# Performance work log

Hardware: AMD Instinct MI355X
Metric: run time of the kernel (lower is better)

Reference implementation:

```python
import jax, jax.numpy as jnp
import numpy as np

D = 2048; HQ = 16; HKV = 4; HD = 128
E = 8; F = 2048; FS = 11008; TOPK = 2
B = 2; S = 1024
EPS = 1e-6
NEG = -1e9


def setup_inputs() -> dict:
    key = jax.random.key(0)
    ks = jax.random.split(key, 16)
    p = lambda k, shape: jax.random.normal(k, shape, jnp.float32) * 0.02
    # rotary tables (rotate-half convention): [S, HD]
    pos = jnp.arange(S, dtype=jnp.float32)[:, None]
    inv = 1.0 / (10000.0 ** (jnp.arange(0, HD, 2, dtype=jnp.float32) / HD))
    ang = pos * inv[None, :]
    cos = jnp.concatenate([jnp.cos(ang), jnp.cos(ang)], axis=-1)
    sin = jnp.concatenate([jnp.sin(ang), jnp.sin(ang)], axis=-1)
    return dict(
        x=jax.random.normal(ks[0], (B, S, D), jnp.float32),
        rope_cos=cos, rope_sin=sin,
        attn_norm_w=jnp.ones((D,), jnp.float32),
        ffn_norm_w=jnp.ones((D,), jnp.float32),
        wq=p(ks[1], (D, HQ * HD)), bq=jnp.zeros((HQ * HD,), jnp.float32),
        wk=p(ks[2], (D, HKV * HD)), bk=jnp.zeros((HKV * HD,), jnp.float32),
        wv=p(ks[3], (D, HKV * HD)), bv=jnp.zeros((HKV * HD,), jnp.float32),
        wo=p(ks[4], (HQ * HD, D)),
        router_w=p(ks[5], (D, E)),
        w_gate=p(ks[6], (E, D, F)), w_up=p(ks[7], (E, D, F)), w_down=p(ks[8], (E, F, D)),
        ws_gate=p(ks[9], (D, FS)), ws_up=p(ks[10], (D, FS)), ws_down=p(ks[11], (FS, D)),
    )


def rmsnorm(x, w):
    return x * jax.lax.rsqrt(jnp.mean(x * x, axis=-1, keepdims=True) + EPS) * w


def rotate_half(x):
    x1, x2 = jnp.split(x, 2, axis=-1)
    return jnp.concatenate([-x2, x1], axis=-1)


def reference(x, rope_cos, rope_sin, attn_norm_w, ffn_norm_w,
              wq, bq, wk, bk, wv, bv, wo, router_w,
              w_gate, w_up, w_down, ws_gate, ws_up, ws_down):
    b, s, d = x.shape
    # ---- attention sublayer ----
    h = rmsnorm(x, attn_norm_w)
    q = (h @ wq + bq).reshape(b, s, HQ, HD)
    k = (h @ wk + bk).reshape(b, s, HKV, HD)
    v = (h @ wv + bv).reshape(b, s, HKV, HD)
    cos = rope_cos[None, :, None, :]
    sin = rope_sin[None, :, None, :]
    q = q * cos + rotate_half(q) * sin
    k = k * cos + rotate_half(k) * sin
    rep = HQ // HKV
    k = jnp.repeat(k, rep, axis=2)   # [b,s,HQ,HD]
    v = jnp.repeat(v, rep, axis=2)
    scores = jnp.einsum('bqhd,bkhd->bhqk', q, k) / np.sqrt(HD).astype(np.float32)
    causal = jnp.tril(jnp.ones((s, s), bool))
    scores = jnp.where(causal[None, None], scores, NEG)
    attn = jax.nn.softmax(scores, axis=-1)
    o = jnp.einsum('bhqk,bkhd->bqhd', attn, v).reshape(b, s, HQ * HD) @ wo
    new_k, new_v = k, v
    x = x + o
    # ---- MoE sublayer ----
    hn = rmsnorm(x, ffn_norm_w).reshape(b * s, d)   # [T,D]
    logits = hn @ router_w                           # [T,E]
    probs = jax.nn.softmax(logits, axis=-1)
    topv, topi = jax.lax.top_k(probs, TOPK)          # [T,K]
    topv = topv / jnp.sum(topv, axis=-1, keepdims=True)
    onehot = jax.nn.one_hot(topi, E, dtype=hn.dtype)  # [T,K,E]
    wdense = jnp.einsum('tke,tk->te', onehot, topv)   # sparse combine weights [T,E]
    g = jnp.einsum('td,edf->tef', hn, w_gate)
    u = jnp.einsum('td,edf->tef', hn, w_up)
    y = jnp.einsum('tef,efd->ted', jax.nn.silu(g) * u, w_down)
    routed = jnp.einsum('ted,te->td', y, wdense)
    shared = (jax.nn.silu(hn @ ws_gate) * (hn @ ws_up)) @ ws_down
    moe = (routed + shared).reshape(b, s, d)
    # load-balancing aux loss (Switch/Mixtral convention)
    frac = jnp.mean(onehot, axis=(0, 1))             # fraction dispatched per expert
    pmean = jnp.mean(probs, axis=0)
    aux_loss = E * jnp.sum(frac * pmean)
    out = x + moe
    return out, (new_k, new_v), aux_loss
```

## Files before the change

### kernel.cpp

```cpp
#include <hip/hip_runtime.h>

typedef unsigned short u16;
typedef unsigned int u32;
typedef unsigned long long u64;
typedef __attribute__((ext_vector_type(4))) unsigned short u16x4;
typedef __attribute__((ext_vector_type(8))) unsigned short u16x8;
typedef __attribute__((ext_vector_type(4))) float f32x4;
typedef __attribute__((ext_vector_type(8))) __bf16 bf16x8;

#define DD 2048
#define TT 2048
#define FSH 11008

__device__ __forceinline__ float bf2f(u16 u) {
  union { u32 i; float f; } v; v.i = ((u32)u) << 16; return v.f;
}
__device__ __forceinline__ u16 f2bf(float f) {
  union { float f; u32 i; } v; v.f = f;
  u32 r = v.i + 0x7fffu + ((v.i >> 16) & 1u);
  return (u16)(r >> 16);
}
__device__ __forceinline__ void gld16(const void* g, void* l) {
  __builtin_amdgcn_global_load_lds((const __attribute__((address_space(1))) void*)g,
                                   (__attribute__((address_space(3))) void*)l, 16, 0, 0);
}

#define MFMA16(d, a, b) d = __builtin_amdgcn_mfma_f32_16x16x32_bf16(a, b, d, 0, 0, 0)

__global__ __launch_bounds__(256) void rmsnorm_k(const float* __restrict__ x,
                                                 const float* __restrict__ w,
                                                 u16* __restrict__ out) {
  const int t = threadIdx.x;
  const float* xr = x + (size_t)blockIdx.x * DD;
  float4 a = *(const float4*)(xr + t * 8);
  float4 b = *(const float4*)(xr + t * 8 + 4);
  float ss = a.x*a.x + a.y*a.y + a.z*a.z + a.w*a.w
           + b.x*b.x + b.y*b.y + b.z*b.z + b.w*b.w;
#pragma unroll
  for (int m = 1; m < 64; m <<= 1) ss += __shfl_xor(ss, m);
  __shared__ float red[4];
  if ((t & 63) == 0) red[t >> 6] = ss;
  __syncthreads();
  float sc = rsqrtf((red[0] + red[1] + red[2] + red[3]) * (1.f / DD) + 1e-6f);
  float4 wa = *(const float4*)(w + t * 8);
  float4 wb = *(const float4*)(w + t * 8 + 4);
  u16x8 o;
  o[0] = f2bf(a.x * sc * wa.x); o[1] = f2bf(a.y * sc * wa.y);
  o[2] = f2bf(a.z * sc * wa.z); o[3] = f2bf(a.w * sc * wa.w);
  o[4] = f2bf(b.x * sc * wb.x); o[5] = f2bf(b.y * sc * wb.y);
  o[6] = f2bf(b.z * sc * wb.z); o[7] = f2bf(b.w * sc * wb.w);
  *(u16x8*)(out + (size_t)blockIdx.x * DD + t * 8) = o;
}

__global__ __launch_bounds__(256) void transp_k(const float* __restrict__ W,
                                                u16* __restrict__ Wt, int R, int C) {
  __shared__ u16 tile[64 * 80];
  const size_t msz = (size_t)R * C;
  const float* Wm = W + msz * blockIdx.z;
  u16* Wtm = Wt + msz * blockIdx.z;
  const int t = threadIdx.x;
  const int n0 = blockIdx.x * 64, k0 = blockIdx.y * 64;
#pragma unroll
  for (int p = 0; p < 4; ++p) {
    const int kk = (t >> 4) + p * 16;
    const int nn = (t & 15) * 4;
    float4 v = *(const float4*)(Wm + (size_t)(k0 + kk) * C + n0 + nn);
    tile[(nn + 0) * 80 + kk] = f2bf(v.x);
    tile[(nn + 1) * 80 + kk] = f2bf(v.y);
    tile[(nn + 2) * 80 + kk] = f2bf(v.z);
    tile[(nn + 3) * 80 + kk] = f2bf(v.w);
  }
  __syncthreads();
#pragma unroll
  for (int p = 0; p < 2; ++p) {
    const int n = (t >> 3) + p * 32;
    const int c = t & 7;
    u16x8 v = *(const u16x8*)(tile + n * 80 + c * 8);
    *(u16x8*)(Wtm + (size_t)(n0 + n) * R + k0 + c * 8) = v;
  }
}

template <int EPI, bool EXPERT, bool INDIR, bool SPLITK>
__global__ __launch_bounds__(256) void gemm2(
    const u16* __restrict__ A, const u16* __restrict__ Bt, void* __restrict__ Cp,
    const void* __restrict__ aux, const float* __restrict__ slotw,
    const int* __restrict__ slot_tok, const int* __restrict__ tiletab,
    int M, int N, int K, int Kc) {
  __shared__ u16 lA[128 * 32];
  __shared__ u16 lB[128 * 32];
  const int t = threadIdx.x, w = t >> 6, l = t & 63;
  const int n0 = blockIdx.x * 128;
  int m0;
  if constexpr (EXPERT) {
    const int ntil = tiletab[0];
    if ((int)blockIdx.y >= ntil) return;
    const int e = tiletab[1 + blockIdx.y * 2];
    m0 = tiletab[2 + blockIdx.y * 2];
    Bt += (size_t)e * N * K;
  } else {
    m0 = blockIdx.y * 128;
  }
  int kbase = 0, KC = K;
  if constexpr (SPLITK) { kbase = blockIdx.z * Kc; KC = Kc; }
  const int srow = w * 16 + (l >> 2);
  const int scol = (l & 3) * 8;
  const int r0 = m0 + srow, r1 = m0 + srow + 64;
  const u16 *ag0, *ag1;
  if constexpr (INDIR) {
    ag0 = A + (size_t)slot_tok[r0] * K + scol + kbase;
    ag1 = A + (size_t)slot_tok[r1] * K + scol + kbase;
  } else {
    ag0 = A + (size_t)r0 * K + scol + kbase;
    ag1 = A + (size_t)r1 * K + scol + kbase;
  }
  const u16* bg0 = Bt + (size_t)(n0 + srow) * K + scol + kbase;
  const u16* bg1 = Bt + (size_t)(n0 + srow + 64) * K + scol + kbase;
  u16* la = lA + w * 512;
  u16* lb = lB + w * 512;
  const int l15 = l & 15, l4 = l >> 4;
  const int wm = w >> 1, wn = w & 1;
  const int fa = (wm * 64 + l15) * 32 + l4 * 8;
  const int fb = (wn * 64 + l15) * 32 + l4 * 8;
  f32x4 acc[4][4] = {};
  for (int ko = 0; ko < KC; ko += 32) {
    __syncthreads();
    gld16(ag0 + ko, la);
    gld16(ag1 + ko, la + 2048);
    gld16(bg0 + ko, lb);
    gld16(bg1 + ko, lb + 2048);
    asm volatile("s_waitcnt vmcnt(0)" ::: "memory");
    __syncthreads();
    bf16x8 af[4], bf[4];
#pragma unroll
    for (int i = 0; i < 4; ++i) {
      af[i] = *(const bf16x8*)(lA + fa + i * 512);
      bf[i] = *(const bf16x8*)(lB + fb + i * 512);
    }
#pragma unroll
    for (int mi = 0; mi < 4; ++mi)
#pragma unroll
      for (int ni = 0; ni < 4; ++ni)
        MFMA16(acc[mi][ni], af[mi], bf[ni]);
  }
  float* Cf = (float*)Cp;
  if constexpr (SPLITK) Cf += (size_t)blockIdx.z * M * N;
#pragma unroll
  for (int mi = 0; mi < 4; ++mi) {
#pragma unroll
    for (int r = 0; r < 4; ++r) {
      const int row = m0 + wm * 64 + mi * 16 + l4 * 4 + r;
#pragma unroll
      for (int ni = 0; ni < 4; ++ni) {
        const int col = n0 + wn * 64 + ni * 16 + l15;
        const size_t idx = (size_t)row * N + col;
        const float v = acc[mi][ni][r];
        if constexpr (EPI == 0) Cf[idx] = v;
        else if constexpr (EPI == 2) ((u16*)Cp)[idx] = f2bf(v);
        else if constexpr (EPI == 3) {
          const float g = bf2f(((const u16*)aux)[idx]);
          ((u16*)Cp)[idx] = f2bf(v * g / (1.f + __expf(-g)));
        } else {
          ((u16*)Cp)[idx] = f2bf(slotw[row] * v);
        }
      }
    }
  }
}

template <int EPI, bool SPLITK>
__global__ __launch_bounds__(512, 2) void gemm8(
    const u16* __restrict__ A, const u16* __restrict__ Bt, void* __restrict__ Cp,
    const u16* __restrict__ aux, int M, int N, int K, int Kc) {
  __shared__ char lds[131072];
  const int t = threadIdx.x, w = t >> 6, l = t & 63;
  const int gx = gridDim.x, gy = gridDim.y;
  const int nwg = gx * gy;
  int wg = blockIdx.y * gx + blockIdx.x;
  wg = (wg & 7) * (nwg >> 3) + (wg >> 3);
  const int m0 = (wg % gy) * 256;
  const int n0 = (wg / gy) * 256;
  int kbase = 0, KC = K;
  if constexpr (SPLITK) {
    kbase = blockIdx.z * Kc;
    const int rem = K - kbase;
    KC = rem < Kc ? rem : Kc;
  }
  const int ktiles = KC >> 6;
  const int wm = w >> 2, wn = w & 3;
  const int l15 = l & 15, l4 = l >> 4;
  const int sro = l >> 3, sc = l & 7;

  const u16* sgp[2][2][2];
  u32 sdo[2][2][2];
#pragma unroll
  for (int isB = 0; isB < 2; ++isB)
#pragma unroll
    for (int h = 0; h < 2; ++h)
#pragma unroll
      for (int i = 0; i < 2; ++i) {
        const int q = i * 8 + w;
        const int r0 = isB ? (((q >> 2) << 6) + h * 32 + (q & 3) * 8)
                           : (((q & 8) << 4) + h * 64 + (q & 7) * 8);
        const int r = r0 + sro;
        const int cl = sc ^ (r & 7);
        const u16* base = isB ? (Bt + (size_t)(n0 + r) * K) : (A + (size_t)(m0 + r) * K);
        sgp[isB][h][i] = base + kbase + cl * 8;
        sdo[isB][h][i] = (u32)(isB * 32768 + r0 * 128);
      }
  auto stage = [&](int b, int isB, int h, int kt) {
    const int kk = kt < ktiles ? kt : ktiles - 1;
#pragma unroll
    for (int i = 0; i < 2; ++i)
      gld16(sgp[isB][h][i] + kk * 64, lds + b * 65536 + sdo[isB][h][i]);
  };
  auto ldA = [&](int b, int mi, int ks) {
    const int row = wm * 128 + mi * 16 + l15;
    const int ch = (ks * 4 + l4) ^ (row & 7);
    return *(const bf16x8*)(lds + b * 65536 + row * 128 + ch * 16);
  };
  auto ldB = [&](int b, int ni, int ks) {
    const int row = wn * 64 + ni * 16 + l15;
    const int ch = (ks * 4 + l4) ^ (row & 7);
    return *(const bf16x8*)(lds + b * 65536 + 32768 + row * 128 + ch * 16);
  };

  f32x4 acc[8][4] = {};
  bf16x8 aR[4][2], b0[2][2], b1[2][2];

  stage(0, 0, 0, 0); stage(0, 1, 0, 0); stage(0, 1, 1, 0); stage(0, 0, 1, 0);
  stage(1, 0, 0, 1); stage(1, 1, 1, 1); stage(1, 0, 1, 1);
  asm volatile("s_waitcnt vmcnt(6)" ::: "memory");
  __builtin_amdgcn_s_barrier();

  for (int kt = 0; kt < ktiles; kt += 2) {
#pragma unroll
    for (int mi = 0; mi < 4; ++mi) { aR[mi][0] = ldA(0, mi, 0); aR[mi][1] = ldA(0, mi, 1); }
#pragma unroll
    for (int ni = 0; ni < 2; ++ni) { b0[ni][0] = ldB(0, ni, 0); b0[ni][1] = ldB(0, ni, 1); }
    stage(1, 1, 0, kt + 1);
    __builtin_amdgcn_s_barrier();
    asm volatile("s_waitcnt lgkmcnt(0)" ::: "memory");
    __builtin_amdgcn_s_setprio(1);
#pragma unroll
    for (int mi = 0; mi < 4; ++mi)
#pragma unroll
      for (int ni = 0; ni < 2; ++ni) {
        MFMA16(acc[mi][ni], aR[mi][0], b0[ni][0]);
        MFMA16(acc[mi][ni], aR[mi][1], b0[ni][1]);
      }
    __builtin_amdgcn_s_setprio(0);
    __builtin_amdgcn_s_barrier();
#pragma unroll
    for (int ni = 0; ni < 2; ++ni) { b1[ni][0] = ldB(0, ni + 2, 0); b1[ni][1] = ldB(0, ni + 2, 1); }
    stage(0, 0, 0, kt + 2);
    __builtin_amdgcn_s_barrier();
    asm volatile("s_waitcnt lgkmcnt(0)" ::: "memory");
    __builtin_amdgcn_s_setprio(1);
#pragma unroll
    for (int mi = 0; mi < 4; ++mi)
#pragma unroll
      for (int ni = 0; ni < 2; ++ni) {
        MFMA16(acc[mi][ni + 2], aR[mi][0], b1[ni][0]);
        MFMA16(acc[mi][ni + 2], aR[mi][1], b1[ni][1]);
      }
    __builtin_amdgcn_s_setprio(0);
    __builtin_amdgcn_s_barrier();
#pragma unroll
    for (int mi = 0; mi < 4; ++mi) { aR[mi][0] = ldA(0, mi + 4, 0); aR[mi][1] = ldA(0, mi + 4, 1); }
    stage(0, 1, 1, kt + 2);
    __builtin_amdgcn_s_barrier();
    asm volatile("s_waitcnt lgkmcnt(0)" ::: "memory");
    __builtin_amdgcn_s_setprio(1);
#pragma unroll
    for (int mi = 0; mi < 4; ++mi)
#pragma unroll
      for (int ni = 0; ni < 2; ++ni) {
        MFMA16(acc[mi + 4][ni + 2], aR[mi][0], b1[ni][0]);
        MFMA16(acc[mi + 4][ni + 2], aR[mi][1], b1[ni][1]);
      }
    __builtin_amdgcn_s_setprio(0);
    __builtin_amdgcn_s_barrier();
    stage(0, 0, 1, kt + 2);
    __builtin_amdgcn_s_barrier();
    __builtin_amdgcn_s_setprio(1);
#pragma unroll
    for (int mi = 0; mi < 4; ++mi)
#pragma unroll
      for (int ni = 0; ni < 2; ++ni) {
        MFMA16(acc[mi + 4][ni], aR[mi][0], b0[ni][0]);
        MFMA16(acc[mi + 4][ni], aR[mi][1], b0[ni][1]);
      }
    __builtin_amdgcn_s_setprio(0);
    asm volatile("s_waitcnt vmcnt(6)" ::: "memory");
    __builtin_amdgcn_s_barrier();
#pragma unroll
    for (int mi = 0; mi < 4; ++mi) { aR[mi][0] = ldA(1, mi, 0); aR[mi][1] = ldA(1, mi, 1); }
#pragma unroll
    for (int ni = 0; ni < 2; ++ni) { b0[ni][0] = ldB(1, ni, 0); b0[ni][1] = ldB(1, ni, 1); }
    stage(0, 1, 0, kt + 2);
    __builtin_amdgcn_s_barrier();
    asm volatile("s_waitcnt lgkmcnt(0)" ::: "memory");
    __builtin_amdgcn_s_setprio(1);
#pragma unroll
    for (int mi = 0; mi < 4; ++mi)
#pragma unroll
      for (int ni = 0; ni < 2; ++ni) {
        MFMA16(acc[mi][ni], aR[mi][0], b0[ni][0]);
        MFMA16(acc[mi][ni], aR[mi][1], b0[ni][1]);
      }
    __builtin_amdgcn_s_setprio(0);
    __builtin_amdgcn_s_barrier();
#pragma unroll
    for (int ni = 0; ni < 2; ++ni) { b1[ni][0] = ldB(1, ni + 2, 0); b1[ni][1] = ldB(1, ni + 2, 1); }
    stage(1, 0, 0, kt + 3);
    __builtin_amdgcn_s_barrier();
    asm volatile("s_waitcnt lgkmcnt(0)" ::: "memory");
    __builtin_amdgcn_s_setprio(1);
#pragma unroll
    for (int mi = 0; mi < 4; ++mi)
#pragma unroll
      for (int ni = 0; ni < 2; ++ni) {
// ... 116 lines not shown
  };
  auto ldB = [&](int b, int mat, int ni, int ks) {
    const int row = wn * 32 + ni * 16 + l15;
    const int ch = (ks * 4 + l4) ^ (row & 7);
    return *(const bf16x8*)(lds + b * 65536 + 32768 + mat * 16384 + row * 128 + ch * 16);
  };

  f32x4 accg[8][2] = {}, accu[8][2] = {};
  bf16x8 aR[4][2], bg[2][2], bu[2][2];

  stgA(0, 0, 0); stgB(0, 0, 0); stgB(0, 1, 0); stgA(0, 1, 0);
  stgA(1, 0, 1); stgB(1, 1, 1); stgA(1, 1, 1);
  asm volatile("s_waitcnt vmcnt(6)" ::: "memory");
  __builtin_amdgcn_s_barrier();

  for (int kt = 0; kt < ktiles; kt += 2) {
#pragma unroll
    for (int mi = 0; mi < 4; ++mi) { aR[mi][0] = ldA(0, mi, 0); aR[mi][1] = ldA(0, mi, 1); }
#pragma unroll
    for (int ni = 0; ni < 2; ++ni) { bg[ni][0] = ldB(0, 0, ni, 0); bg[ni][1] = ldB(0, 0, ni, 1); }
    stgB(1, 0, kt + 1);
    __builtin_amdgcn_s_barrier();
    asm volatile("s_waitcnt lgkmcnt(0)" ::: "memory");
    __builtin_amdgcn_s_setprio(1);
#pragma unroll
    for (int mi = 0; mi < 4; ++mi)
#pragma unroll
      for (int ni = 0; ni < 2; ++ni) {
        MFMA16(accg[mi][ni], aR[mi][0], bg[ni][0]);
        MFMA16(accg[mi][ni], aR[mi][1], bg[ni][1]);
      }
    __builtin_amdgcn_s_setprio(0);
    __builtin_amdgcn_s_barrier();
#pragma unroll
    for (int ni = 0; ni < 2; ++ni) { bu[ni][0] = ldB(0, 1, ni, 0); bu[ni][1] = ldB(0, 1, ni, 1); }
    stgA(0, 0, kt + 2);
    __builtin_amdgcn_s_barrier();
    asm volatile("s_waitcnt lgkmcnt(0)" ::: "memory");
    __builtin_amdgcn_s_setprio(1);
#pragma unroll
    for (int mi = 0; mi < 4; ++mi)
#pragma unroll
      for (int ni = 0; ni < 2; ++ni) {
        MFMA16(accu[mi][ni], aR[mi][0], bu[ni][0]);
        MFMA16(accu[mi][ni], aR[mi][1], bu[ni][1]);
      }
    __builtin_amdgcn_s_setprio(0);
    __builtin_amdgcn_s_barrier();
#pragma unroll
    for (int mi = 0; mi < 4; ++mi) { aR[mi][0] = ldA(0, mi + 4, 0); aR[mi][1] = ldA(0, mi + 4, 1); }
    stgB(0, 1, kt + 2);
    __builtin_amdgcn_s_barrier();
    asm volatile("s_waitcnt lgkmcnt(0)" ::: "memory");
    __builtin_amdgcn_s_setprio(1);
#pragma unroll
    for (int mi = 0; mi < 4; ++mi)
#pragma unroll
      for (int ni = 0; ni < 2; ++ni) {
        MFMA16(accu[mi + 4][ni], aR[mi][0], bu[ni][0]);
        MFMA16(accu[mi + 4][ni], aR[mi][1], bu[ni][1]);
      }
    __builtin_amdgcn_s_setprio(0);
    __builtin_amdgcn_s_barrier();
    stgA(0, 1, kt + 2);
    __builtin_amdgcn_s_barrier();
    __builtin_amdgcn_s_setprio(1);
#pragma unroll
    for (int mi = 0; mi < 4; ++mi)
#pragma unroll
      for (int ni = 0; ni < 2; ++ni) {
        MFMA16(accg[mi + 4][ni], aR[mi][0], bg[ni][0]);
        MFMA16(accg[mi + 4][ni], aR[mi][1], bg[ni][1]);
      }
    __builtin_amdgcn_s_setprio(0);
    asm volatile("s_waitcnt vmcnt(6)" ::: "memory");
    __builtin_amdgcn_s_barrier();
#pragma unroll
    for (int mi = 0; mi < 4; ++mi) { aR[mi][0] = ldA(1, mi, 0); aR[mi][1] = ldA(1, mi, 1); }
#pragma unroll
    for (int ni = 0; ni < 2; ++ni) { bg[ni][0] = ldB(1, 0, ni, 0); bg[ni][1] = ldB(1, 0, ni, 1); }
    stgB(0, 0, kt + 2);
    __builtin_amdgcn_s_barrier();
    asm volatile("s_waitcnt lgkmcnt(0)" ::: "memory");
    __builtin_amdgcn_s_setprio(1);
#pragma unroll
    for (int mi = 0; mi < 4; ++mi)
#pragma unroll
      for (int ni = 0; ni < 2; ++ni) {
        MFMA16(accg[mi][ni], aR[mi][0], bg[ni][0]);
        MFMA16(accg[mi][ni], aR[mi][1], bg[ni][1]);
      }
    __builtin_amdgcn_s_setprio(0);
    __builtin_amdgcn_s_barrier();
#pragma unroll
    for (int ni = 0; ni < 2; ++ni) { bu[ni][0] = ldB(1, 1, ni, 0); bu[ni][1] = ldB(1, 1, ni, 1); }
    stgA(1, 0, kt + 3);
    __builtin_amdgcn_s_barrier();
    asm volatile("s_waitcnt lgkmcnt(0)" ::: "memory");
    __builtin_amdgcn_s_setprio(1);
#pragma unroll
    for (int mi = 0; mi < 4; ++mi)
#pragma unroll
      for (int ni = 0; ni < 2; ++ni) {
        MFMA16(accu[mi][ni], aR[mi][0], bu[ni][0]);
        MFMA16(accu[mi][ni], aR[mi][1], bu[ni][1]);
      }
    __builtin_amdgcn_s_setprio(0);
    __builtin_amdgcn_s_barrier();
#pragma unroll
    for (int mi = 0; mi < 4; ++mi) { aR[mi][0] = ldA(1, mi + 4, 0); aR[mi][1] = ldA(1, mi + 4, 1); }
    stgB(1, 1, kt + 3);
    __builtin_amdgcn_s_barrier();
    asm volatile("s_waitcnt lgkmcnt(0)" ::: "memory");
    __builtin_amdgcn_s_setprio(1);
#pragma unroll
    for (int mi = 0; mi < 4; ++mi)
#pragma unroll
      for (int ni = 0; ni < 2; ++ni) {
        MFMA16(accu[mi + 4][ni], aR[mi][0], bu[ni][0]);
        MFMA16(accu[mi + 4][ni], aR[mi][1], bu[ni][1]);
      }
    __builtin_amdgcn_s_setprio(0);
    __builtin_amdgcn_s_barrier();
    stgA(1, 1, kt + 3);
    __builtin_amdgcn_s_barrier();
    __builtin_amdgcn_s_setprio(1);
#pragma unroll
    for (int mi = 0; mi < 4; ++mi)
#pragma unroll
      for (int ni = 0; ni < 2; ++ni) {
        MFMA16(accg[mi + 4][ni], aR[mi][0], bg[ni][0]);
        MFMA16(accg[mi + 4][ni], aR[mi][1], bg[ni][1]);
      }
    __builtin_amdgcn_s_setprio(0);
    asm volatile("s_waitcnt vmcnt(6)" ::: "memory");
    __builtin_amdgcn_s_barrier();
  }

#pragma unroll
  for (int mi = 0; mi < 8; ++mi)
#pragma unroll
    for (int rr = 0; rr < 4; ++rr) {
      const int row = m0 + wm * 128 + mi * 16 + l4 * 4 + rr;
#pragma unroll
      for (int ni = 0; ni < 2; ++ni) {
        const int col = cg0 + nt * 128 + wn * 32 + ni * 16 + l15;
        const float g = accg[mi][ni][rr];
        const float u = accu[mi][ni][rr];
        act[(size_t)row * LDC + col] = f2bf(u * g / (1.f + __expf(-g)));
      }
    }
}

template <int NP, bool ADDB>
__global__ __launch_bounds__(256) void red_k(float* __restrict__ dst,
                                             const float* __restrict__ base,
                                             const float* __restrict__ parts,
                                             int mn4) {
  const int i = blockIdx.x * 256 + threadIdx.x;
  float4 s;
  if constexpr (ADDB) s = ((const float4*)base)[i];
  else { s.x = s.y = s.z = s.w = 0.f; }
#pragma unroll
  for (int p = 0; p < NP; ++p) {
    const float4 v = ((const float4*)parts)[(size_t)p * mn4 + i];
    s.x += v.x; s.y += v.y; s.z += v.z; s.w += v.w;
  }
  ((float4*)dst)[i] = s;
}

__global__ __launch_bounds__(256) void redbf_k(float* __restrict__ dst,
                                               const float* __restrict__ base,
                                               const u16* __restrict__ parts) {
  const int i = blockIdx.x * 256 + threadIdx.x;
  float s[8];
  const float* bp = base + (size_t)i * 8;
#pragma unroll
  for (int j = 0; j < 8; ++j) s[j] = bp[j];
#pragma unroll
  for (int p = 0; p < 4; ++p) {
    u16x8 v = ((const u16x8*)parts)[(size_t)p * 524288 + i];
#pragma unroll
    for (int j = 0; j < 8; ++j) s[j] += bf2f(v[j]);
  }
  float* dp = dst + (size_t)i * 8;
#pragma unroll
  for (int j = 0; j < 8; ++j) dp[j] = s[j];
}

__global__ __launch_bounds__(256) void rope_k(
    const float* __restrict__ p0, const float* __restrict__ p1,
    const float* __restrict__ cosb, const float* __restrict__ sinb,
    const float* __restrict__ bq, const float* __restrict__ bk, const float* __restrict__ bv,
    u16* __restrict__ QR, u16* __restrict__ KR, u16* __restrict__ VB,
    float* __restrict__ NK, float* __restrict__ NV) {
  const int s = blockIdx.x, b = blockIdx.y, t = threadIdx.x;
  const size_t tok = (size_t)b * 1024 + s;
  const float* r0 = p0 + tok * 3072;
  const float* r1 = p1 + tok * 3072;
  const float* cr = cosb + s * 128;
  const float* sr = sinb + s * 128;
  for (int i = t; i < 1024; i += 256) {
    const int h = i >> 6, d = i & 63;
    const float v1 = r0[h * 128 + d] + r1[h * 128 + d] + bq[h * 128 + d];
    const float v2 = r0[h * 128 + d + 64] + r1[h * 128 + d + 64] + bq[h * 128 + d + 64];
    const float o1 = v1 * cr[d] - v2 * sr[d];
    const float o2 = v2 * cr[d + 64] + v1 * sr[d + 64];
    const size_t qb = (((size_t)(b * 16 + h)) * 1024 + s) * 128;
    QR[qb + d] = f2bf(o1);
    QR[qb + d + 64] = f2bf(o2);
  }
  {
    const int h = t >> 6, d = t & 63;
    const float v1 = r0[2048 + h * 128 + d] + r1[2048 + h * 128 + d] + bk[h * 128 + d];
    const float v2 = r0[2048 + h * 128 + d + 64] + r1[2048 + h * 128 + d + 64] + bk[h * 128 + d + 64];
    const float o1 = v1 * cr[d] - v2 * sr[d];
    const float o2 = v2 * cr[d + 64] + v1 * sr[d + 64];
    const size_t kb = (((size_t)(b * 4 + h)) * 1024 + s) * 128;
    KR[kb + d] = f2bf(o1);
    KR[kb + d + 64] = f2bf(o2);
    const size_t ob = tok * 2048;
#pragma unroll
    for (int rep = 0; rep < 4; ++rep) {
      NK[ob + (h * 4 + rep) * 128 + d] = o1;
      NK[ob + (h * 4 + rep) * 128 + d + 64] = o2;
    }
  }
  for (int i = t; i < 512; i += 256) {
    const int h = i >> 7, d = i & 127;
    const float v = r0[2560 + i] + r1[2560 + i] + bv[i];
    VB[(((size_t)(b * 4 + h)) * 1024 + s) * 128 + d] = f2bf(v);
    const size_t ob = tok * 2048;
#pragma unroll
    for (int rep = 0; rep < 4; ++rep) NV[ob + (h * 4 + rep) * 128 + d] = v;
  }
}

__global__ __launch_bounds__(256) void attn_k(const u16* __restrict__ Q,
                                              const u16* __restrict__ Kc,
                                              const u16* __restrict__ Vc,
                                              u16* __restrict__ O) {
  const int qt = blockIdx.x, h = blockIdx.y, b = blockIdx.z;
  const int t = threadIdx.x, w = t >> 6, l = t & 63;
  const int kvh = h >> 2;
  __shared__ u16 Ks[64 * 128];
  __shared__ u16 Vt[128 * 66];
  __shared__ u16 Ps[4][16 * 68];
  const int l15 = l & 15, l4 = l >> 4;
  bf16x8 qf[4];
  {
    const u16* qb = Q + (((size_t)(b * 16 + h)) * 1024 + qt * 64 + w * 16 + l15) * 128 + l4 * 8;
#pragma unroll
    for (int c = 0; c < 4; ++c) qf[c] = *(const bf16x8*)(qb + c * 32);
  }
  float m_run[4] = {-1e30f, -1e30f, -1e30f, -1e30f};
  float l_run[4] = {0.f, 0.f, 0.f, 0.f};
  f32x4 accO[8] = {};
  const size_t kvbase = ((size_t)(b * 4 + kvh)) * 1024 * 128;
  const int ntiles = qt + 1;
  for (int kt = 0; kt < ntiles; ++kt) {
    __syncthreads();
    {
      const int key = t >> 2;
      const u16* kg = Kc + kvbase + (size_t)(kt * 64 + key) * 128;
      const u16* vg = Vc + kvbase + (size_t)(kt * 64 + key) * 128;
      const int sw = (key & 7) << 4;
#pragma unroll
      for (int p = 0; p < 4; ++p) {
        const int ch = (t & 3) * 4 + p;
        *(u16x8*)((char*)Ks + key * 256 + ((ch * 16) ^ sw)) = *(const u16x8*)(kg + ch * 8);
        const int d0 = ch * 8;
        u16x8 vv = *(const u16x8*)(vg + d0);
#pragma unroll
        for (int j = 0; j < 8; ++j) Vt[(d0 + j) * 66 + key] = vv[j];
      }
    }
    __syncthreads();
    f32x4 sf[4] = {};
#pragma unroll
    for (int nf = 0; nf < 4; ++nf) {
      const int keyl = nf * 16 + l15;
      const int sw = (keyl & 7) << 4;
      const char* kbase = (const char*)Ks + keyl * 256;
#pragma unroll
      for (int c = 0; c < 4; ++c) {
        bf16x8 kf = *(const bf16x8*)(kbase + ((c * 64 + l4 * 16) ^ sw));
        sf[nf] = __builtin_amdgcn_mfma_f32_16x16x32_bf16(qf[c], kf, sf[nf], 0, 0, 0);
      }
    }
    const int qg0 = qt * 64 + w * 16 + l4 * 4;
    float alpha[4];
#pragma unroll
    for (int r = 0; r < 4; ++r) {
      const int qg = qg0 + r;
      float tm = -1e30f;
#pragma unroll
      for (int nf = 0; nf < 4; ++nf) {
        const int kg = kt * 64 + nf * 16 + l15;
        float sv = sf[nf][r] * 0.088388347648318447f;
        sv = (kg <= qg) ? sv : -1e30f;
        sf[nf][r] = sv;
        tm = fmaxf(tm, sv);
      }
#pragma unroll
      for (int mm = 1; mm < 16; mm <<= 1) tm = fmaxf(tm, __shfl_xor(tm, mm));
      const float mn = fmaxf(m_run[r], tm);
      alpha[r] = __expf(m_run[r] - mn);
      m_run[r] = mn;
      float rs = 0.f;
#pragma unroll
      for (int nf = 0; nf < 4; ++nf) {
        const float p = __expf(sf[nf][r] - mn);
        sf[nf][r] = p;
        rs += p;
      }
#pragma unroll
      for (int mm = 1; mm < 16; mm <<= 1) rs += __shfl_xor(rs, mm);
      l_run[r] = l_run[r] * alpha[r] + rs;
    }
#pragma unroll
    for (int nf = 0; nf < 8; ++nf)
#pragma unroll
      for (int r = 0; r < 4; ++r) accO[nf][r] *= alpha[r];
#pragma unroll
    for (int nf = 0; nf < 4; ++nf)
#pragma unroll
      for (int r = 0; r < 4; ++r)
        Ps[w][(l4 * 4 + r) * 68 + nf * 16 + l15] = f2bf(sf[nf][r]);
    __syncthreads();
#pragma unroll
    for (int kc = 0; kc < 2; ++kc) {
      const u16* pb = &Ps[w][0] + l15 * 68 + kc * 32 + l4 * 8;
      union { u16x4 q[2]; bf16x8 v; } pu;
      pu.q[0] = *(const u16x4*)pb;
      pu.q[1] = *(const u16x4*)(pb + 4);
#pragma unroll
      for (int nf = 0; nf < 8; ++nf) {
        const int dd = nf * 16 + l15;
        const u16* vp = &Vt[0] + dd * 66 + kc * 32 + l4 * 8;
        union { u32 u[4]; bf16x8 v; } vu;
        vu.u[0] = *(const u32*)(vp);
        vu.u[1] = *(const u32*)(vp + 2);
        vu.u[2] = *(const u32*)(vp + 4);
        vu.u[3] = *(const u32*)(vp + 6);
        accO[nf] = __builtin_amdgcn_mfma_f32_16x16x32_bf16(pu.v, vu.v, accO[nf], 0, 0, 0);
      }
    }
  }
  const int qg0 = qt * 64 + w * 16 + l4 * 4;
#pragma unroll
  for (int nf = 0; nf < 8; ++nf) {
    const int dd = nf * 16 + l15;
#pragma unroll
    for (int r = 0; r < 4; ++r) {
      const float o = accO[nf][r] / l_run[r];
      O[((size_t)(b * 1024 + qg0 + r)) * 2048 + h * 128 + dd] = f2bf(o);
    }
  }
}

__global__ __launch_bounds__(256) void router_k(
    const float* __restrict__ x2, const float* __restrict__ wn, const float* __restrict__ rw,
    int* __restrict__ topi2, float* __restrict__ topw2,
    int* __restrict__ counts, u64* __restrict__ pmean) {
  const int t = threadIdx.x, w = t >> 6, l = t & 63;
  const int tok = blockIdx.x * 4 + w;
  __shared__ int lc[8];
  __shared__ u64 lp[8];
  if (t < 8) { lc[t] = 0; lp[t] = 0ull; }
  __syncthreads();
  const float* xr = x2 + (size_t)tok * DD;
  float ss = 0.f;
#pragma unroll
  for (int i = 0; i < 8; ++i) {
    float4 v = *(const float4*)(xr + l * 32 + i * 4);
    ss += v.x * v.x + v.y * v.y + v.z * v.z + v.w * v.w;
  }
#pragma unroll
  for (int m = 1; m < 64; m <<= 1) ss += __shfl_xor(ss, m);
  const float sc = rsqrtf(ss * (1.f / DD) + 1e-6f);
  float acc[8] = {};
  for (int i = 0; i < 32; ++i) {
    const int d = l * 32 + i;
    const float hv = xr[d] * sc * wn[d];
    float4 r0 = *(const float4*)(rw + d * 8);
    float4 r1 = *(const float4*)(rw + d * 8 + 4);
    acc[0] += hv * r0.x; acc[1] += hv * r0.y; acc[2] += hv * r0.z; acc[3] += hv * r0.w;
    acc[4] += hv * r1.x; acc[5] += hv * r1.y; acc[6] += hv * r1.z; acc[7] += hv * r1.w;
  }
#pragma unroll
  for (int m = 1; m < 64; m <<= 1)
#pragma unroll
    for (int e = 0; e < 8; ++e) acc[e] += __shfl_xor(acc[e], m);
  if (l == 0) {
    float mx = acc[0];
#pragma unroll
    for (int e = 1; e < 8; ++e) mx = fmaxf(mx, acc[e]);
    float p[8], sum = 0.f;
#pragma unroll
    for (int e = 0; e < 8; ++e) { p[e] = __expf(acc[e] - mx); sum += p[e]; }
    const float inv = 1.f / sum;
#pragma unroll
    for (int e = 0; e < 8; ++e) p[e] *= inv;
    int e0 = 0; float v0 = p[0];
#pragma unroll
    for (int e = 1; e < 8; ++e) if (p[e] > v0) { v0 = p[e]; e0 = e; }
    int e1 = (e0 == 0) ? 1 : 0; float v1 = p[e1];
#pragma unroll
    for (int e = 0; e < 8; ++e) if (e != e0 && p[e] > v1) { v1 = p[e]; e1 = e; }
    const float wsum = v0 + v1;
    topi2[tok * 2] = e0; topi2[tok * 2 + 1] = e1;
    topw2[tok * 2] = v0 / wsum; topw2[tok * 2 + 1] = v1 / wsum;
    atomicAdd(&lc[e0], 1); atomicAdd(&lc[e1], 1);
#pragma unroll
    for (int e = 0; e < 8; ++e) atomicAdd(&lp[e], (u64)((double)p[e] * 4294967296.0));
  }
  __syncthreads();
  if (t < 8) {
    if (lc[t]) atomicAdd(&counts[t], lc[t]);
    if (lp[t]) atomicAdd(&pmean[t], lp[t]);
  }
}

__global__ __launch_bounds__(256) void zero_k(int* __restrict__ counts, u64* __restrict__ pmean,
                                              int* __restrict__ slot_tok, float* __restrict__ slot_w) {
  const int i = blockIdx.x * 256 + threadIdx.x;
  if (i < 5120) { slot_tok[i] = 0; slot_w[i] = 0.f; }
  if (i < 8) { counts[i] = 0; pmean[i] = 0ull; }
}

__global__ void scan_k(const int* __restrict__ counts, int* __restrict__ cursors,
                       int* __restrict__ tiletab, const u64* __restrict__ pmean,
                       float* __restrict__ auxout) {
  if (threadIdx.x == 0) {
    int off = 0, nt = 0;
    double aux = 0.0;
    for (int e = 0; e < 8; ++e) {
      cursors[e] = off;
      const int c = counts[e];
      const int nte = (c + 127) >> 7;
      for (int i = 0; i < nte; ++i) {
        tiletab[1 + nt * 2] = e;
        tiletab[2 + nt * 2] = off + i * 128;
        ++nt;
      }
      off += nte * 128;
      const double pm = ((double)pmean[e] / 4294967296.0) / 2048.0;
      aux += ((double)c / 4096.0) * pm;
    }
    tiletab[0] = nt;
    *auxout = (float)(8.0 * aux);
  }
}

__global__ __launch_bounds__(256) void assign_k(const int* __restrict__ topi2,
                                                const float* __restrict__ topw2,
                                                int* __restrict__ cursors,
                                                int* __restrict__ slot_tok,
                                                float* __restrict__ slot_w,
                                                int* __restrict__ tok_slot) {
  const int tok = blockIdx.x * 256 + threadIdx.x;
#pragma unroll
  for (int j = 0; j < 2; ++j) {
    const int e = topi2[tok * 2 + j];
    const int s = atomicAdd(&cursors[e], 1);
    slot_tok[s] = tok;
    slot_w[s] = topw2[tok * 2 + j];
    tok_slot[tok * 2 + j] = s;
  }
}

__global__ __launch_bounds__(256) void final_k(float* __restrict__ out,
                                               const u16* __restrict__ routed,
                                               const int* __restrict__ tok_slot) {
  const int tok = blockIdx.x, t = threadIdx.x;
  const int s0 = tok_slot[tok * 2], s1 = tok_slot[tok * 2 + 1];
  u16x8 a = ((const u16x8*)(routed + (size_t)s0 * DD))[t];
  u16x8 b = ((const u16x8*)(routed + (size_t)s1 * DD))[t];
  float* o = out + (size_t)tok * DD + t * 8;
  float4 o0 = *(const float4*)o;
  float4 o1 = *(const float4*)(o + 4);
  o0.x += bf2f(a[0]) + bf2f(b[0]); o0.y += bf2f(a[1]) + bf2f(b[1]);
  o0.z += bf2f(a[2]) + bf2f(b[2]); o0.w += bf2f(a[3]) + bf2f(b[3]);
  o1.x += bf2f(a[4]) + bf2f(b[4]); o1.y += bf2f(a[5]) + bf2f(b[5]);
  o1.z += bf2f(a[6]) + bf2f(b[6]); o1.w += bf2f(a[7]) + bf2f(b[7]);
  *(float4*)o = o0;
  *(float4*)(o + 4) = o1;
}

extern "C" void kernel_launch(void* const* d_in, const int* in_sizes, int n_in,
                              void* d_out, int out_size, void* d_ws, size_t ws_size,
                              hipStream_t stream) {
  (void)in_sizes; (void)n_in; (void)out_size; (void)ws_size;
  const float* x    = (const float*)d_in[0];
  const float* rc   = (const float*)d_in[1];
  const float* rs   = (const float*)d_in[2];
  const float* anw  = (const float*)d_in[3];
  const float* fnw  = (const float*)d_in[4];
  const float* wq   = (const float*)d_in[5];
  const float* bq   = (const float*)d_in[6];
  const float* wk   = (const float*)d_in[7];
  const float* bk   = (const float*)d_in[8];
  const float* wv   = (const float*)d_in[9];
  const float* bv   = (const float*)d_in[10];
  const float* wo   = (const float*)d_in[11];
  const float* rw   = (const float*)d_in[12];
  const float* wg   = (const float*)d_in[13];
  const float* wu   = (const float*)d_in[14];
  const float* wd   = (const float*)d_in[15];
  const float* wsg  = (const float*)d_in[16];
  const float* wsu  = (const float*)d_in[17];
  const float* wsd  = (const float*)d_in[18];

  const size_t MB = (size_t)1 << 20;
  char* ws = (char*)d_ws;
  float* X2  = (float*)(ws + 0);
  u16*   HN  = (u16*)(ws + 16 * MB);
  char*  SM  = ws + 24 * MB;
  char*  AR  = ws + 25 * MB;

  int*   CNT   = (int*)(SM);
  u64*   PM    = (u64*)(SM + 64);
  int*   CURS  = (int*)(SM + 256);
  int*   TILT  = (int*)(SM + 512);
  int*   TOPI  = (int*)(SM + 4096);
  float* TOPW  = (float*)(SM + 40960);
  int*   STOK  = (int*)(SM + 73728);
  float* SW    = (float*)(SM + 98304);
  int*   TSLOT = (int*)(SM + 131072);

  u16*   H      = (u16*)(AR);
  u16*   WTQ    = (u16*)(AR + 8 * MB);
  float* PARTSQ = (float*)(AR + 20 * MB);
  u16*   ATTNO = (u16*)(AR);
  u16*   QR    = (u16*)(AR + 68 * MB);
  u16*   KR    = (u16*)(AR + 76 * MB);
  u16*   VBb   = (u16*)(AR + 78 * MB);
  u16*   WTO    = (u16*)(AR + 8 * MB);
  float* PARTSW = (float*)(AR + 16 * MB);
  u16*   G      = (u16*)(AR);
  u16*   WTSg   = (u16*)(AR + 43 * MB);
  u16*   WTSu   = (u16*)(AR + 59 * MB);
  u16*   WTSd   = (u16*)(AR + 43 * MB);
  u16*   PARTSD = (u16*)(AR + 86 * MB);
  u16*   WTE    = (u16*)(AR);
  u16*   GEXP   = (u16*)(AR + 64 * MB);
  u16*   ROUTED = (u16*)(AR + 84 * MB);

  float* out  = (float*)d_out;
  float* NK   = out + 4194304;
  float* NV   = out + 2 * 4194304;
  float* AUXO = out + 3 * 4194304;

  const dim3 b256(256);
  const dim3 b512(512);

  rmsnorm_k<<<TT, b256, 0, stream>>>(x, anw, H);
  transp_k<<<dim3(32, 32, 1), b256, 0, stream>>>(wq, WTQ, 2048, 2048);
  transp_k<<<dim3(8, 32, 1), b256, 0, stream>>>(wk, WTQ + (size_t)2048 * 2048, 2048, 512);
  transp_k<<<dim3(8, 32, 1), b256, 0, stream>>>(wv, WTQ + (size_t)2560 * 2048, 2048, 512);
  gemm8<11, true><<<dim3(12, 8, 2), b512, 0, stream>>>(H, WTQ, PARTSQ, nullptr, TT, 3072, 2048, 1024);
  rope_k<<<dim3(1024, 2), b256, 0, stream>>>(PARTSQ, PARTSQ + (size_t)TT * 3072, rc, rs,
                                             bq, bk, bv, QR, KR, VBb, NK, NV);
  attn_k<<<dim3(16, 16, 2), b256, 0, stream>>>(QR, KR, VBb, ATTNO);
  transp_k<<<dim3(32, 32, 1), b256, 0, stream>>>(wo, WTO, 2048, 2048);
  gemm8<11, true><<<dim3(8, 8, 4), b512, 0, stream>>>(ATTNO, WTO, PARTSW, nullptr, TT, 2048, 2048, 512);
  red_k<4, true><<<4096, b256, 0, stream>>>(X2, x, PARTSW, 1048576);
  rmsnorm_k<<<TT, b256, 0, stream>>>(X2, fnw, HN);
  zero_k<<<20, b256, 0, stream>>>(CNT, PM, STOK, SW);
  router_k<<<512, b256, 0, stream>>>(X2, fnw, rw, TOPI, TOPW, CNT, PM);
  scan_k<<<1, 64, 0, stream>>>(CNT, CURS, TILT, PM, AUXO);
  assign_k<<<8, b256, 0, stream>>>(TOPI, TOPW, CURS, STOK, SW, TSLOT);
  {
    const int cg[4] = {0, 3712, 7424, 11008};
    for (int gi = 0; gi < 3; ++gi) {
      const int c0 = cg[gi], wgrp = cg[gi + 1] - c0, ngc = wgrp >> 7;
      transp_k<<<dim3(wgrp / 64, 32, 1), b256, 0, stream>>>(wsg + c0, WTSg, 2048, FSH);
      transp_k<<<dim3(wgrp / 64, 32, 1), b256, 0, stream>>>(wsu + c0, WTSu, 2048, FSH);
      gemm_gu<<<dim3(ngc, 8, 1), b512, 0, stream>>>(HN, WTSg, WTSu, G, 2048, FSH, c0);
    }
  }
  transp_k<<<dim3(32, 172, 1), b256, 0, stream>>>(wsd, WTSd, FSH, 2048);
  gemm8<10, true><<<dim3(8, 8, 4), b512, 0, stream>>>(G, WTSd, PARTSD, nullptr, TT, 2048, FSH, 2816);
  redbf_k<<<2048, b256, 0, stream>>>(out, X2, PARTSD);
  transp_k<<<dim3(32, 32, 8), b256, 0, stream>>>(wg, WTE, 2048, 2048);
  gemm2<2, true, true, false><<<dim3(16, 40, 1), b256, 0, stream>>>(
      HN, WTE, GEXP, nullptr, nullptr, STOK, TILT, 5120, 2048, 2048, 0);
  transp_k<<<dim3(32, 32, 8), b256, 0, stream>>>(wu, WTE, 2048, 2048);
  gemm2<3, true, true, false><<<dim3(16, 40, 1), b256, 0, stream>>>(
      HN, WTE, GEXP, GEXP, nullptr, STOK, TILT, 5120, 2048, 2048, 0);
  transp_k<<<dim3(32, 32, 8), b256, 0, stream>>>(wd, WTE, 2048, 2048);
  gemm2<4, true, false, false><<<dim3(16, 40, 1), b256, 0, stream>>>(
      GEXP, WTE, ROUTED, nullptr, SW, STOK, TILT, 5120, 2048, 2048, 0);
  final_k<<<TT, b256, 0, stream>>>(out, ROUTED, TSLOT);
}
```

Measured before the change: 936.2 us.

## Fuse expert gate/up GEMMs, fuse residual+norm+router, bf16 QKV partials, attn setprio

Adds a fused expert gate/up GEMM that computes both projections per tile and applies SiLU-mul in the epilogue, processing experts in two halves so both transposed weight sets fit in scratch. The residual reduction, RMSNorm and router are merged into one kernel, which removes two launches and extra passes over X2. QKV split-K partials are stored as bf16 instead of fp32 to halve traffic into rope_k, and the attention MFMA sections are raised in wave priority with s_setprio. Risks include lower precision in the QKV partials, global atomics per token in the router, and a simple non-pipelined GEMM loop in the new gate/up kernel.

```diff
diff --git a/kernel.cpp b/kernel.cpp
--- a/kernel.cpp
+++ b/kernel.cpp
@@ -167,6 +167,84 @@
   }
 }
 
+__global__ __launch_bounds__(512) void gemm2gu(
+    const u16* __restrict__ A, const u16* __restrict__ Btg, const u16* __restrict__ Btu,
+    u16* __restrict__ act, const int* __restrict__ slot_tok, const int* __restrict__ tiletab,
+    int N, int K, int ebase) {
+  __shared__ u16 SH[16384];
+  const int t = threadIdx.x, w = t >> 6, l = t & 63;
+  const int n0 = blockIdx.x * 128;
+  const int ntil = tiletab[0];
+  if ((int)blockIdx.y >= ntil) return;
+  const int e = tiletab[1 + blockIdx.y * 2];
+  if (e < ebase || e >= ebase + 4) return;
+  const int m0 = tiletab[2 + blockIdx.y * 2];
+  const size_t boff = (size_t)(e - ebase) * N * K;
+  const u16* Bg = Btg + boff;
+  const u16* Bu = Btu + boff;
+  const int srow = w * 16 + (l >> 2);
+  const int scol = (l & 3) * 8;
+  const u16* ag = A + (size_t)slot_tok[m0 + srow] * K + scol;
+  const u16* bgp = Bg + (size_t)(n0 + srow) * K + scol;
+  const u16* bup = Bu + (size_t)(n0 + srow) * K + scol;
+  u16* la = SH + w * 512;
+  u16* lbg = SH + 4096 + w * 512;
+  u16* lbu = SH + 8192 + w * 512;
+  const int l15 = l & 15, l4 = l >> 4;
+  const int wm = w >> 2, wn = w & 3;
+  const int mat = wn >> 1, ch = wn & 1;
+  const int fa = (wm * 64 + l15) * 32 + l4 * 8;
+  const int fb = (mat ? 8192 : 4096) + (ch * 64 + l15) * 32 + l4 * 8;
+  f32x4 acc[4][4] = {};
+  for (int ko = 0; ko < K; ko += 32) {
+    __syncthreads();
+    gld16(ag + ko, la);
+    gld16(bgp + ko, lbg);
+    gld16(bup + ko, lbu);
+    asm volatile("s_waitcnt vmcnt(0)" ::: "memory");
+    __syncthreads();
+    bf16x8 af[4], bf[4];
+#pragma unroll
+    for (int i = 0; i < 4; ++i) {
+      af[i] = *(const bf16x8*)(SH + fa + i * 512);
+      bf[i] = *(const bf16x8*)(SH + fb + i * 512);
+    }
+#pragma unroll
+    for (int mi = 0; mi < 4; ++mi)
+#pragma unroll
+      for (int ni = 0; ni < 4; ++ni)
+        MFMA16(acc[mi][ni], af[mi], bf[ni]);
+  }
+  __syncthreads();
+  if (mat == 0) {
+    u16* gr = SH + (wm * 2 + ch) * 4096;
+#pragma unroll
+    for (int mi = 0; mi < 4; ++mi)
+#pragma unroll
+      for (int r = 0; r < 4; ++r)
+#pragma unroll
+        for (int ni = 0; ni < 4; ++ni)
+          gr[(mi * 16 + l4 * 4 + r) * 64 + ni * 16 + l15] = f2bf(acc[mi][ni][r]);
+  }
+  __syncthreads();
+  if (mat == 1) {
+    const u16* gr = SH + (wm * 2 + ch) * 4096;
+#pragma unroll
+    for (int mi = 0; mi < 4; ++mi)
+#pragma unroll
+      for (int r = 0; r < 4; ++r) {
+        const int row = m0 + wm * 64 + mi * 16 + l4 * 4 + r;
+#pragma unroll
+        for (int ni = 0; ni < 4; ++ni) {
+          const float g = bf2f(gr[(mi * 16 + l4 * 4 + r) * 64 + ni * 16 + l15]);
+          const float u = acc[mi][ni][r];
+          act[(size_t)row * N + n0 + ch * 64 + ni * 16 + l15] =
+              f2bf(u * g / (1.f + __expf(-g)));
+        }
+      }
+  }
+}
+
 template <int EPI, bool SPLITK>
 __global__ __launch_bounds__(512, 2) void gemm8(
     const u16* __restrict__ A, const u16* __restrict__ Bt, void* __restrict__ Cp,
@@ -589,23 +667,6 @@
     }
 }
 
-template <int NP, bool ADDB>
-__global__ __launch_bounds__(256) void red_k(float* __restrict__ dst,
-                                             const float* __restrict__ base,
-                                             const float* __restrict__ parts,
-                                             int mn4) {
-  const int i = blockIdx.x * 256 + threadIdx.x;
-  float4 s;
-  if constexpr (ADDB) s = ((const float4*)base)[i];
-  else { s.x = s.y = s.z = s.w = 0.f; }
-#pragma unroll
-  for (int p = 0; p < NP; ++p) {
-    const float4 v = ((const float4*)parts)[(size_t)p * mn4 + i];
-    s.x += v.x; s.y += v.y; s.z += v.z; s.w += v.w;
-  }
-  ((float4*)dst)[i] = s;
-}
-
 __global__ __launch_bounds__(256) void redbf_k(float* __restrict__ dst,
                                                const float* __restrict__ base,
                                                const u16* __restrict__ parts) {
@@ -626,21 +687,21 @@
 }
 
 __global__ __launch_bounds__(256) void rope_k(
-    const float* __restrict__ p0, const float* __restrict__ p1,
+    const u16* __restrict__ p0, const u16* __restrict__ p1,
     const float* __restrict__ cosb, const float* __restrict__ sinb,
     const float* __restrict__ bq, const float* __restrict__ bk, const float* __restrict__ bv,
     u16* __restrict__ QR, u16* __restrict__ KR, u16* __restrict__ VB,
     float* __restrict__ NK, float* __restrict__ NV) {
   const int s = blockIdx.x, b = blockIdx.y, t = threadIdx.x;
   const size_t tok = (size_t)b * 1024 + s;
-  const float* r0 = p0 + tok * 3072;
-  const float* r1 = p1 + tok * 3072;
+  const u16* r0 = p0 + tok * 3072;
+  const u16* r1 = p1 + tok * 3072;
   const float* cr = cosb + s * 128;
   const float* sr = sinb + s * 128;
   for (int i = t; i < 1024; i += 256) {
     const int h = i >> 6, d = i & 63;
-    const float v1 = r0[h * 128 + d] + r1[h * 128 + d] + bq[h * 128 + d];
-    const float v2 = r0[h * 128 + d + 64] + r1[h * 128 + d + 64] + bq[h * 128 + d + 64];
+    const float v1 = bf2f(r0[h * 128 + d]) + bf2f(r1[h * 128 + d]) + bq[h * 128 + d];
+    const float v2 = bf2f(r0[h * 128 + d + 64]) + bf2f(r1[h * 128 + d + 64]) + bq[h * 128 + d + 64];
     const float o1 = v1 * cr[d] - v2 * sr[d];
     const float o2 = v2 * cr[d + 64] + v1 * sr[d + 64];
     const size_t qb = (((size_t)(b * 16 + h)) * 1024 + s) * 128;
@@ -649,8 +710,8 @@
   }
   {
     const int h = t >> 6, d = t & 63;
-    const float v1 = r0[2048 + h * 128 + d] + r1[2048 + h * 128 + d] + bk[h * 128 + d];
-    const float v2 = r0[2048 + h * 128 + d + 64] + r1[2048 + h * 128 + d + 64] + bk[h * 128 + d + 64];
+    const float v1 = bf2f(r0[2048 + h * 128 + d]) + bf2f(r1[2048 + h * 128 + d]) + bk[h * 128 + d];
+    const float v2 = bf2f(r0[2048 + h * 128 + d + 64]) + bf2f(r1[2048 + h * 128 + d + 64]) + bk[h * 128 + d + 64];
     const float o1 = v1 * cr[d] - v2 * sr[d];
     const float o2 = v2 * cr[d + 64] + v1 * sr[d + 64];
     const size_t kb = (((size_t)(b * 4 + h)) * 1024 + s) * 128;
@@ -665,7 +726,7 @@
   }
   for (int i = t; i < 512; i += 256) {
     const int h = i >> 7, d = i & 127;
-    const float v = r0[2560 + i] + r1[2560 + i] + bv[i];
+    const float v = bf2f(r0[2560 + i]) + bf2f(r1[2560 + i]) + bv[i];
     VB[(((size_t)(b * 4 + h)) * 1024 + s) * 128 + d] = f2bf(v);
     const size_t ob = tok * 2048;
 #pragma unroll
@@ -714,6 +775,7 @@
     }
     __syncthreads();
     f32x4 sf[4] = {};
+    __builtin_amdgcn_s_setprio(1);
 #pragma unroll
     for (int nf = 0; nf < 4; ++nf) {
       const int keyl = nf * 16 + l15;
@@ -725,6 +787,7 @@
         sf[nf] = __builtin_amdgcn_mfma_f32_16x16x32_bf16(qf[c], kf, sf[nf], 0, 0, 0);
       }
     }
+    __builtin_amdgcn_s_setprio(0);
     const int qg0 = qt * 64 + w * 16 + l4 * 4;
     float alpha[4];
 #pragma unroll
@@ -765,6 +828,7 @@
       for (int r = 0; r < 4; ++r)
         Ps[w][(l4 * 4 + r) * 68 + nf * 16 + l15] = f2bf(sf[nf][r]);
     __syncthreads();
+    __builtin_amdgcn_s_setprio(1);
 #pragma unroll
     for (int kc = 0; kc < 2; ++kc) {
       const u16* pb = &Ps[w][0] + l15 * 68 + kc * 32 + l4 * 8;
@@ -783,6 +847,7 @@
         accO[nf] = __builtin_amdgcn_mfma_f32_16x16x32_bf16(pu.v, vu.v, accO[nf], 0, 0, 0);
       }
     }
+    __builtin_amdgcn_s_setprio(0);
   }
   const int qg0 = qt * 64 + w * 16 + l4 * 4;
 #pragma unroll
@@ -796,46 +861,77 @@
   }
 }
 
-__global__ __launch_bounds__(256) void router_k(
-    const float* __restrict__ x2, const float* __restrict__ wn, const float* __restrict__ rw,
+__global__ __launch_bounds__(256) void fuserouter_k(
+    const float* __restrict__ x, const float* __restrict__ parts,
+    const float* __restrict__ wn, const float* __restrict__ rw,
+    float* __restrict__ X2, u16* __restrict__ HN,
     int* __restrict__ topi2, float* __restrict__ topw2,
     int* __restrict__ counts, u64* __restrict__ pmean) {
-  const int t = threadIdx.x, w = t >> 6, l = t & 63;
-  const int tok = blockIdx.x * 4 + w;
-  __shared__ int lc[8];
-  __shared__ u64 lp[8];
-  if (t < 8) { lc[t] = 0; lp[t] = 0ull; }
+  const int t = threadIdx.x, w = t >> 6;
+  const int tok = blockIdx.x;
+  const size_t base = (size_t)tok * DD + t * 8;
+  float v[8];
+  {
+    float4 a = *(const float4*)(x + base);
+    float4 b = *(const float4*)(x + base + 4);
+    v[0] = a.x; v[1] = a.y; v[2] = a.z; v[3] = a.w;
+    v[4] = b.x; v[5] = b.y; v[6] = b.z; v[7] = b.w;
+  }
+#pragma unroll
+  for (int p = 0; p < 4; ++p) {
+    const float* pr = parts + (size_t)p * (TT * DD) + base;
+    float4 a = *(const float4*)(pr);
+    float4 b = *(const float4*)(pr + 4);
+    v[0] += a.x; v[1] += a.y; v[2] += a.z; v[3] += a.w;
+    v[4] += b.x; v[5] += b.y; v[6] += b.z; v[7] += b.w;
+  }
+  *(float4*)(X2 + base) = make_float4(v[0], v[1], v[2], v[3]);
+  *(float4*)(X2 + base + 4) = make_float4(v[4], v[5], v[6], v[7]);
+  float ss = 0.f;
+#pragma unroll
+  for (int j = 0; j < 8; ++j) ss += v[j] * v[j];
+#pragma unroll
+  for (int m = 1; m < 64; m <<= 1) ss += __shfl_xor(ss, m);
+  __shared__ float red[4];
+  __shared__ float racc[32];
+  if ((t & 63) == 0) red[w] = ss;
   __syncthreads();
-  const float* xr = x2 + (size_t)tok * DD;
-  float ss = 0.f;
-#pragma unroll
-  for (int i = 0; i < 8; ++i) {
-    float4 v = *(const float4*)(xr + l * 32 + i * 4);
-    ss += v.x * v.x + v.y * v.y + v.z * v.z + v.w * v.w;
-  }
-#pragma unroll
-  for (int m = 1; m < 64; m <<= 1) ss += __shfl_xor(ss, m);
-  const float sc = rsqrtf(ss * (1.f / DD) + 1e-6f);
+  const float sc = rsqrtf((red[0] + red[1] + red[2] + red[3]) * (1.f / DD) + 1e-6f);
+  float hn[8];
+  u16x8 o;
+#pragma unroll
+  for (int j = 0; j < 8; ++j) {
+    hn[j] = v[j] * sc * wn[t * 8 + j];
+    o[j] = f2bf(hn[j]);
+  }
+  *(u16x8*)(HN + base) = o;
   float acc[8] = {};
-  for (int i = 0; i < 32; ++i) {
-    const int d = l * 32 + i;
-    const float hv = xr[d] * sc * wn[d];
+#pragma unroll
+  for (int j = 0; j < 8; ++j) {
+    const int d = t * 8 + j;
     float4 r0 = *(const float4*)(rw + d * 8);
     float4 r1 = *(const float4*)(rw + d * 8 + 4);
-    acc[0] += hv * r0.x; acc[1] += hv * r0.y; acc[2] += hv * r0.z; acc[3] += hv * r0.w;
-    acc[4] += hv * r1.x; acc[5] += hv * r1.y; acc[6] += hv * r1.z; acc[7] += hv * r1.w;
+    acc[0] += hn[j] * r0.x; acc[1] += hn[j] * r0.y; acc[2] += hn[j] * r0.z; acc[3] += hn[j] * r0.w;
+    acc[4] += hn[j] * r1.x; acc[5] += hn[j] * r1.y; acc[6] += hn[j] * r1.z; acc[7] += hn[j] * r1.w;
   }
 #pragma unroll
   for (int m = 1; m < 64; m <<= 1)
 #pragma unroll
     for (int e = 0; e < 8; ++e) acc[e] += __shfl_xor(acc[e], m);
-  if (l == 0) {
-    float mx = acc[0];
-#pragma unroll
-    for (int e = 1; e < 8; ++e) mx = fmaxf(mx, acc[e]);
+  if ((t & 63) == 0)
+#pragma unroll
+    for (int e = 0; e < 8; ++e) racc[w * 8 + e] = acc[e];
+  __syncthreads();
+  if (t == 0) {
+    float lg[8];
+#pragma unroll
+    for (int e = 0; e < 8; ++e) lg[e] = racc[e] + racc[8 + e] + racc[16 + e] + racc[24 + e];
+    float mx = lg[0];
+#pragma unroll
+    for (int e = 1; e < 8; ++e) mx = fmaxf(mx, lg[e]);
     float p[8], sum = 0.f;
 #pragma unroll
-    for (int e = 0; e < 8; ++e) { p[e] = __expf(acc[e] - mx); sum += p[e]; }
+    for (int e = 0; e < 8; ++e) { p[e] = __expf(lg[e] - mx); sum += p[e]; }
     const float inv = 1.f / sum;
 #pragma unroll
     for (int e = 0; e < 8; ++e) p[e] *= inv;
@@ -848,14 +944,9 @@
     const float wsum = v0 + v1;
     topi2[tok * 2] = e0; topi2[tok * 2 + 1] = e1;
     topw2[tok * 2] = v0 / wsum; topw2[tok * 2 + 1] = v1 / wsum;
-    atomicAdd(&lc[e0], 1); atomicAdd(&lc[e1], 1);
-#pragma unroll
-    for (int e = 0; e < 8; ++e) atomicAdd(&lp[e], (u64)((double)p[e] * 4294967296.0));
-  }
-  __syncthreads();
-  if (t < 8) {
-    if (lc[t]) atomicAdd(&counts[t], lc[t]);
-    if (lp[t]) atomicAdd(&pmean[t], lp[t]);
+    atomicAdd(&counts[e0], 1); atomicAdd(&counts[e1], 1);
+#pragma unroll
+    for (int e = 0; e < 8; ++e) atomicAdd(&pmean[e], (u64)((double)p[e] * 4294967296.0));
   }
 }
 
@@ -968,7 +1059,7 @@
 
   u16*   H      = (u16*)(AR);
   u16*   WTQ    = (u16*)(AR + 8 * MB);
-  float* PARTSQ = (float*)(AR + 20 * MB);
+  u16*   PARTSQ = (u16*)(AR + 20 * MB);
   u16*   ATTNO = (u16*)(AR);
   u16*   QR    = (u16*)(AR + 68 * MB);
   u16*   KR    = (u16*)(AR + 76 * MB);
@@ -980,9 +1071,11 @@
   u16*   WTSu   = (u16*)(AR + 59 * MB);
   u16*   WTSd   = (u16*)(AR + 43 * MB);
   u16*   PARTSD = (u16*)(AR + 86 * MB);
-  u16*   WTE    = (u16*)(AR);
-  u16*   GEXP   = (u16*)(AR + 64 * MB);
+  u16*   WTEg   = (u16*)(AR);
+  u16*   WTEu   = (u16*)(AR + 32 * MB);
+  u16*   ACT    = (u16*)(AR + 64 * MB);
   u16*   ROUTED = (u16*)(AR + 84 * MB);
+  u16*   WTEd   = (u16*)(AR);
 
   float* out  = (float*)d_out;
   float* NK   = out + 4194304;
@@ -996,16 +1089,14 @@
   transp_k<<<dim3(32, 32, 1), b256, 0, stream>>>(wq, WTQ, 2048, 2048);
   transp_k<<<dim3(8, 32, 1), b256, 0, stream>>>(wk, WTQ + (size_t)2048 * 2048, 2048, 512);
   transp_k<<<dim3(8, 32, 1), b256, 0, stream>>>(wv, WTQ + (size_t)2560 * 2048, 2048, 512);
-  gemm8<11, true><<<dim3(12, 8, 2), b512, 0, stream>>>(H, WTQ, PARTSQ, nullptr, TT, 3072, 2048, 1024);
+  gemm8<10, true><<<dim3(12, 8, 2), b512, 0, stream>>>(H, WTQ, PARTSQ, nullptr, TT, 3072, 2048, 1024);
   rope_k<<<dim3(1024, 2), b256, 0, stream>>>(PARTSQ, PARTSQ + (size_t)TT * 3072, rc, rs,
                                              bq, bk, bv, QR, KR, VBb, NK, NV);
   attn_k<<<dim3(16, 16, 2), b256, 0, stream>>>(QR, KR, VBb, ATTNO);
   transp_k<<<dim3(32, 32, 1), b256, 0, stream>>>(wo, WTO, 2048, 2048);
   gemm8<11, true><<<dim3(8, 8, 4), b512, 0, stream>>>(ATTNO, WTO, PARTSW, nullptr, TT, 2048, 2048, 512);
-  red_k<4, true><<<4096, b256, 0, stream>>>(X2, x, PARTSW, 1048576);
-  rmsnorm_k<<<TT, b256, 0, stream>>>(X2, fnw, HN);
   zero_k<<<20, b256, 0, stream>>>(CNT, PM, STOK, SW);
-  router_k<<<512, b256, 0, stream>>>(X2, fnw, rw, TOPI, TOPW, CNT, PM);
+  fuserouter_k<<<TT, b256, 0, stream>>>(x, PARTSW, fnw, rw, X2, HN, TOPI, TOPW, CNT, PM);
   scan_k<<<1, 64, 0, stream>>>(CNT, CURS, TILT, PM, AUXO);
   assign_k<<<8, b256, 0, stream>>>(TOPI, TOPW, CURS, STOK, SW, TSLOT);
   {
@@ -1020,14 +1111,14 @@
   transp_k<<<dim3(32, 172, 1), b256, 0, stream>>>(wsd, WTSd, FSH, 2048);
   gemm8<10, true><<<dim3(8, 8, 4), b512, 0, stream>>>(G, WTSd, PARTSD, nullptr, TT, 2048, FSH, 2816);
   redbf_k<<<2048, b256, 0, stream>>>(out, X2, PARTSD);
-  transp_k<<<dim3(32, 32, 8), b256, 0, stream>>>(wg, WTE, 2048, 2048);
-  gemm2<2, true, true, false><<<dim3(16, 40, 1), b256, 0, stream>>>(
-      HN, WTE, GEXP, nullptr, nullptr, STOK, TILT, 5120, 2048, 2048, 0);
-  transp_k<<<dim3(32, 32, 8), b256, 0, stream>>>(wu, WTE, 2048, 2048);
-  gemm2<3, true, true, false><<<dim3(16, 40, 1), b256, 0, stream>>>(
-      HN, WTE, GEXP, GEXP, nullptr, STOK, TILT, 5120, 2048, 2048, 0);
-  transp_k<<<dim3(32, 32, 8), b256, 0, stream>>>(wd, WTE, 2048, 2048);
+  for (int cb = 0; cb < 2; ++cb) {
+    const int eb = cb * 4;
+    transp_k<<<dim3(32, 32, 4), b256, 0, stream>>>(wg + (size_t)eb * 2048 * 2048, WTEg, 2048, 2048);
+    transp_k<<<dim3(32, 32, 4), b256, 0, stream>>>(wu + (size_t)eb * 2048 * 2048, WTEu, 2048, 2048);
+    gemm2gu<<<dim3(16, 40, 1), b512, 0, stream>>>(HN, WTEg, WTEu, ACT, STOK, TILT, 2048, 2048, eb);
+  }
+  transp_k<<<dim3(32, 32, 8), b256, 0, stream>>>(wd, WTEd, 2048, 2048);
   gemm2<4, true, false, false><<<dim3(16, 40, 1), b256, 0, stream>>>(
-      GEXP, WTE, ROUTED, nullptr, SW, STOK, TILT, 5120, 2048, 2048, 0);
+      ACT, WTEd, ROUTED, nullptr, SW, STOK, TILT, 5120, 2048, 2048, 0);
   final_k<<<TT, b256, 0, stream>>>(out, ROUTED, TSLOT);
 }
```

Measured after the change: 1.116 ms. +19.2%, slower.
